# Kernel optimization log

Measured on AMD Instinct MI355X. Metric: run time of the kernel, lower is better.

Reference implementation:

```python
import jax, jax.numpy as jnp
import numpy as np

N_NODES = 100000
N_EDGES = 1600000
HIDDEN = 64


def gcn_conv(x, edge_index, W, b):
    """PyG GCNConv: add self-loops, symmetric deg^{-1/2} normalization, scatter-add."""
    n = x.shape[0]
    h = x @ W  # [N, F_out]
    loop = jnp.arange(n, dtype=edge_index.dtype)
    src = jnp.concatenate([edge_index[0], loop])  # [E+N]
    dst = jnp.concatenate([edge_index[1], loop])
    deg = jax.ops.segment_sum(jnp.ones_like(dst, dtype=h.dtype), dst, num_segments=n)
    dinv = jnp.where(deg > 0, jax.lax.rsqrt(jnp.maximum(deg, 1e-12)), 0.0)
    norm = dinv[src] * dinv[dst]  # [E+N]
    msg = h[src] * norm[:, None]  # gather + scale
    out = jax.ops.segment_sum(msg, dst, num_segments=n)  # scatter-add
    return out + b


def setup_inputs() -> dict:
    key = jax.random.key(0)
    k = jax.random.split(key, 6)
    x = jax.random.normal(k[0], (N_NODES, HIDDEN), dtype=jnp.float32)
    edge_index = jax.random.randint(k[1], (2, N_EDGES), 0, N_NODES, dtype=jnp.int32)
    s = 1.0 / np.sqrt(HIDDEN)
    W1 = jax.random.normal(k[2], (HIDDEN, HIDDEN), dtype=jnp.float32) * s
    b1 = jnp.zeros((HIDDEN,), dtype=jnp.float32)
    W2 = jax.random.normal(k[3], (HIDDEN, HIDDEN), dtype=jnp.float32) * s
    b2 = jnp.zeros((HIDDEN,), dtype=jnp.float32)
    return {"x": x, "edge_index": edge_index, "W1": W1, "b1": b1, "W2": W2, "b2": b2}


def reference(x, edge_index, W1, b1, W2, b2):
    # Faithful to source: conv1 applied twice, relu, dropout (eval -> identity), conv2, log_softmax.
    h = gcn_conv(x, edge_index, W1, b1)
    h = jax.nn.relu(gcn_conv(h, edge_index, W1, b1))
    # F.dropout(training=self.training): identity in eval mode
    h = gcn_conv(h, edge_index, W2, b2)
    return jax.nn.log_softmax(h, axis=1)
```

## Files before the change

### kernel.cpp

```cpp
#include <hip/hip_runtime.h>
#include <hip/hip_bf16.h>

#define HID 64

__device__ __forceinline__ void acc8(float* a, uint4 v) {
    a[0] += __uint_as_float(v.x << 16);
    a[1] += __uint_as_float(v.x & 0xffff0000u);
    a[2] += __uint_as_float(v.y << 16);
    a[3] += __uint_as_float(v.y & 0xffff0000u);
    a[4] += __uint_as_float(v.z << 16);
    a[5] += __uint_as_float(v.z & 0xffff0000u);
    a[6] += __uint_as_float(v.w << 16);
    a[7] += __uint_as_float(v.w & 0xffff0000u);
}


__global__ __launch_bounds__(256) void hist_part_kernel(
    const int* __restrict__ dst, int* __restrict__ cnt, int E, int psz) {
    int part = blockIdx.x & 7, chunk = blockIdx.x >> 3;
    int i = chunk * 256 + threadIdx.x;
    if (i >= E) return;
    int d = dst[i];
    if (d / psz == part) atomicAdd(&cnt[d], 1);
}

__global__ __launch_bounds__(256) void bsum_kernel(const int* __restrict__ cnt,
                                                   int* __restrict__ bsums, int N) {
    __shared__ int s[256];
    int tid = threadIdx.x, i = blockIdx.x * 256 + tid;
    s[tid] = (i < N) ? cnt[i] : 0;
    __syncthreads();
    for (int o = 128; o > 0; o >>= 1) {
        if (tid < o) s[tid] += s[tid + o];
        __syncthreads();
    }
    if (tid == 0) bsums[blockIdx.x] = s[0];
}

__global__ __launch_bounds__(512) void scan_bsums_kernel(int* __restrict__ bsums, int nblk) {
    __shared__ int s[512];
    int tid = threadIdx.x;
    int orig = (tid < nblk) ? bsums[tid] : 0;
    s[tid] = orig;
    __syncthreads();
    for (int off = 1; off < 512; off <<= 1) {
        int v = (tid >= off) ? s[tid - off] : 0;
        __syncthreads();
        s[tid] += v;
        __syncthreads();
    }
    if (tid < nblk) bsums[tid] = s[tid] - orig;
}

__global__ __launch_bounds__(256) void rowptr_kernel(
    const int* __restrict__ cnt, const int* __restrict__ bsums,
    int* __restrict__ row_ptr, int* __restrict__ cursor,
    float* __restrict__ dinv, int N) {
    __shared__ int s[256];
    int tid = threadIdx.x, i = blockIdx.x * 256 + tid;
    int c = (i < N) ? cnt[i] : 0;
    s[tid] = c;
    __syncthreads();
    for (int off = 1; off < 256; off <<= 1) {
        int v = (tid >= off) ? s[tid - off] : 0;
        __syncthreads();
        s[tid] += v;
        __syncthreads();
    }
    if (i < N) {
        int excl = s[tid] - c + bsums[blockIdx.x];
        row_ptr[i] = excl;
        cursor[i]  = excl;
        dinv[i]    = rsqrtf((float)c + 1.0f);
    }
}

__global__ __launch_bounds__(256) void fill_part_kernel(
    const int* __restrict__ src, const int* __restrict__ dst,
    int* __restrict__ cursor, int* __restrict__ col, int E, int psz) {
    int part = blockIdx.x & 7, chunk = blockIdx.x >> 3;
    int i = chunk * 256 + threadIdx.x;
    if (i >= E) return;
    int d = dst[i];
    if (d / psz == part) {
        int p = atomicAdd(&cursor[d], 1);
        col[p] = src[i];
    }
}

__device__ __forceinline__ void gather64(
    const uint4* __restrict__ g4, const int* __restrict__ col,
    int beg, int deg, int n, int N, int lane, float* t) {
    int eighth = lane >> 3, fo = lane & 7;
    float a0[8] = {}, a1[8] = {}, a2[8] = {}, a3[8] = {};
    for (int base = 0; base < deg; base += 64) {
        int rem = deg - base; rem = rem > 64 ? 64 : rem;
        int c = (lane < rem) ? col[beg + base + lane] : N;
        int groups = (rem + 7) >> 3;
        int j = 0;
        for (; j + 4 <= groups; j += 4) {
            int s0 = __shfl(c, 8 * (j + 0) + eighth, 64);
            int s1 = __shfl(c, 8 * (j + 1) + eighth, 64);
            int s2 = __shfl(c, 8 * (j + 2) + eighth, 64);
            int s3 = __shfl(c, 8 * (j + 3) + eighth, 64);
            uint4 v0 = g4[(size_t)s0 * 8 + fo];
            uint4 v1 = g4[(size_t)s1 * 8 + fo];
            uint4 v2 = g4[(size_t)s2 * 8 + fo];
            uint4 v3 = g4[(size_t)s3 * 8 + fo];
            acc8(a0, v0); acc8(a1, v1); acc8(a2, v2); acc8(a3, v3);
        }
        if (j + 2 <= groups) {
            int s0 = __shfl(c, 8 * (j + 0) + eighth, 64);
            int s1 = __shfl(c, 8 * (j + 1) + eighth, 64);
            uint4 v0 = g4[(size_t)s0 * 8 + fo];
            uint4 v1 = g4[(size_t)s1 * 8 + fo];
            acc8(a0, v0); acc8(a1, v1);
            j += 2;
        }
        if (j < groups) {
            int s0 = __shfl(c, 8 * j + eighth, 64);
            uint4 v0 = g4[(size_t)s0 * 8 + fo];
            acc8(a0, v0);
        }
    }
    float sf[8] = {};
    acc8(sf, g4[(size_t)n * 8 + fo]);
#pragma unroll
    for (int k = 0; k < 8; ++k) {
        float s = (a0[k] + a1[k]) + (a2[k] + a3[k]);
        s += __shfl_xor(s, 8, 64);
        s += __shfl_xor(s, 16, 64);
        s += __shfl_xor(s, 32, 64);
        t[k] = s + sf[k];
    }
}


__global__ __launch_bounds__(256) void gemm_scale_kernel(
    const float* __restrict__ X, const float* __restrict__ W,
    const float* __restrict__ dinv, __hip_bfloat16* __restrict__ g, int N) {
    __shared__ float Ws[HID * HID];
    __shared__ float4 xs4[4][HID / 4];
    int tid = threadIdx.x;
    for (int i = tid; i < HID * HID; i += 256) Ws[i] = W[i];
    __syncthreads();
    int w = tid >> 6, c = tid & 63;
    float* xsw = (float*)xs4[w];
    int ngrp = (N + 4) / 4;
    for (int grp = blockIdx.x; grp < ngrp; grp += gridDim.x) {
        int row = grp * 4 + w;
        if (row > N) continue;
        if (row == N) { g[(size_t)N * HID + c] = __float2bfloat16(0.f); continue; }
        xsw[c] = X[(size_t)row * HID + c];
        float acc = 0.f;
#pragma unroll
        for (int k = 0; k < HID; ++k) acc = fmaf(xsw[k], Ws[k * HID + c], acc);
        g[(size_t)row * HID + c] = __float2bfloat16(acc * dinv[row]);
    }
}


template <bool RELU>
__global__ __launch_bounds__(256) void agg_gemm_kernel(
    const __hip_bfloat16* __restrict__ g_in, const int* __restrict__ row_ptr,
    const int* __restrict__ cnt, const int* __restrict__ col,
    const float* __restrict__ dinv, const float* __restrict__ bias,
    const float* __restrict__ W, __hip_bfloat16* __restrict__ g_out, int N) {
    __shared__ float Ws[HID * HID];
    __shared__ float4 xs4[4][HID / 4];
    int tid = threadIdx.x;
    for (int i = tid; i < HID * HID; i += 256) Ws[i] = W[i];
    __syncthreads();
    int w = tid >> 6, lane = tid & 63;
    int eighth = lane >> 3, fo = lane & 7;
    const uint4* g4 = (const uint4*)g_in;
    float* xsw = (float*)xs4[w];
    float bb[8];
#pragma unroll
    for (int k = 0; k < 8; ++k) bb[k] = bias[8 * fo + k];
    int ngrp = (N + 4) / 4;
    for (int grp = blockIdx.x; grp < ngrp; grp += gridDim.x) {
        int n = grp * 4 + w;
        if (n > N) continue;
        if (n == N) { g_out[(size_t)N * HID + lane] = __float2bfloat16(0.f); continue; }
        int beg = __builtin_amdgcn_readfirstlane(row_ptr[n]);
        int deg = __builtin_amdgcn_readfirstlane(cnt[n]);
        float dn = __uint_as_float(__builtin_amdgcn_readfirstlane(__float_as_uint(dinv[n])));
        float t[8];
        gather64(g4, col, beg, deg, n, N, lane, t);
        if (eighth == 0) {
            float4 o0, o1;
            o0.x = fmaf(dn, t[0], bb[0]); o0.y = fmaf(dn, t[1], bb[1]);
            o0.z = fmaf(dn, t[2], bb[2]); o0.w = fmaf(dn, t[3], bb[3]);
            o1.x = fmaf(dn, t[4], bb[4]); o1.y = fmaf(dn, t[5], bb[5]);
            o1.z = fmaf(dn, t[6], bb[6]); o1.w = fmaf(dn, t[7], bb[7]);
            if (RELU) {
                o0.x = fmaxf(o0.x, 0.f); o0.y = fmaxf(o0.y, 0.f);
                o0.z = fmaxf(o0.z, 0.f); o0.w = fmaxf(o0.w, 0.f);
                o1.x = fmaxf(o1.x, 0.f); o1.y = fmaxf(o1.y, 0.f);
                o1.z = fmaxf(o1.z, 0.f); o1.w = fmaxf(o1.w, 0.f);
            }
            xs4[w][2 * fo]     = o0;
            xs4[w][2 * fo + 1] = o1;
        }
        float acc = 0.f;
#pragma unroll
        for (int k = 0; k < HID; ++k) acc = fmaf(xsw[k], Ws[k * HID + lane], acc);
        g_out[(size_t)n * HID + lane] = __float2bfloat16(acc * dn);
    }
}


__global__ __launch_bounds__(256) void agg_lsm_kernel(
    const __hip_bfloat16* __restrict__ g_in, const int* __restrict__ row_ptr,
    const int* __restrict__ cnt, const int* __restrict__ col,
    const float* __restrict__ dinv, const float* __restrict__ bias,
    float* __restrict__ out, int N) {
    int tid = threadIdx.x;
    int n = blockIdx.x * 4 + (tid >> 6);
    if (n >= N) return;
    int lane = tid & 63;
    int eighth = lane >> 3, fo = lane & 7;
    int beg = __builtin_amdgcn_readfirstlane(row_ptr[n]);
    int deg = __builtin_amdgcn_readfirstlane(cnt[n]);
    float dn = __uint_as_float(__builtin_amdgcn_readfirstlane(__float_as_uint(dinv[n])));
    const uint4* g4 = (const uint4*)g_in;
    float t[8];
    gather64(g4, col, beg, deg, n, N, lane, t);
    float v[8];
#pragma unroll
    for (int k = 0; k < 8; ++k) v[k] = fmaf(dn, t[k], bias[8 * fo + k]);
    float mx = v[0];
#pragma unroll
    for (int k = 1; k < 8; ++k) mx = fmaxf(mx, v[k]);
    mx = fmaxf(mx, __shfl_xor(mx, 1, 64));
    mx = fmaxf(mx, __shfl_xor(mx, 2, 64));
    mx = fmaxf(mx, __shfl_xor(mx, 4, 64));
    float sum = 0.f;
#pragma unroll
    for (int k = 0; k < 8; ++k) sum += expf(v[k] - mx);
    sum += __shfl_xor(sum, 1, 64);
    sum += __shfl_xor(sum, 2, 64);
    sum += __shfl_xor(sum, 4, 64);
    float ls = mx + logf(sum);
    if (eighth == 0) {
        float4 o0 = make_float4(v[0] - ls, v[1] - ls, v[2] - ls, v[3] - ls);
        float4 o1 = make_float4(v[4] - ls, v[5] - ls, v[6] - ls, v[7] - ls);
        ((float4*)out)[(size_t)n * 16 + 2 * fo]     = o0;
        ((float4*)out)[(size_t)n * 16 + 2 * fo + 1] = o1;
    }
}


static inline size_t alignup(size_t x) { return (x + 255) & ~(size_t)255; }

extern "C" void kernel_launch(void* const* d_in, const int* in_sizes, int n_in,
                              void* d_out, int out_size, void* d_ws, size_t ws_size,
                              hipStream_t stream) {
    const float* x  = (const float*)d_in[0];
    const int*   ei = (const int*)d_in[1];
    const float* W1 = (const float*)d_in[2];
    const float* b1 = (const float*)d_in[3];
    const float* W2 = (const float*)d_in[4];
    const float* b2 = (const float*)d_in[5];

    const int N = in_sizes[0] / HID;
    const int E = in_sizes[1] / 2;
    const int* src = ei;
    const int* dst = ei + E;

    const int nblk = (N + 255) / 256;
    const int psz  = (N + 7) / 8;

    char* w = (char*)d_ws;
    float*          dinv    = (float*)w;          w += alignup((size_t)N * 4);
    __hip_bfloat16* gA      = (__hip_bfloat16*)w; w += alignup((size_t)(N + 1) * HID * 2);
    __hip_bfloat16* gB      = (__hip_bfloat16*)w; w += alignup((size_t)(N + 1) * HID * 2);
    int*            cnt     = (int*)w;            w += alignup((size_t)N * 4);
    int*            row_ptr = (int*)w;            w += alignup((size_t)N * 4);
    int*            cursor  = (int*)w;            w += alignup((size_t)N * 4);
    int*            col     = (int*)w;            w += alignup((size_t)E * 4);
    int*            bsums   = (int*)w;            w += alignup((size_t)nblk * 4);

    const int egrid = (E + 255) / 256;
    const int ngrid = (N + 3) / 4;
    const int gsgrid = 2048;

    hipMemsetAsync(cnt, 0, (size_t)N * sizeof(int), stream);
    hist_part_kernel<<<egrid * 8, 256, 0, stream>>>(dst, cnt, E, psz);
    bsum_kernel<<<nblk, 256, 0, stream>>>(cnt, bsums, N);
    scan_bsums_kernel<<<1, 512, 0, stream>>>(bsums, nblk);
    rowptr_kernel<<<nblk, 256, 0, stream>>>(cnt, bsums, row_ptr, cursor, dinv, N);
    fill_part_kernel<<<egrid * 8, 256, 0, stream>>>(src, dst, cursor, col, E, psz);

    gemm_scale_kernel<<<gsgrid, 256, 0, stream>>>(x, W1, dinv, gA, N);
    agg_gemm_kernel<false><<<gsgrid, 256, 0, stream>>>(gA, row_ptr, cnt, col, dinv, b1, W1, gB, N);
    agg_gemm_kernel<true><<<gsgrid, 256, 0, stream>>>(gB, row_ptr, cnt, col, dinv, b1, W2, gA, N);
    agg_lsm_kernel<<<ngrid, 256, 0, stream>>>(gA, row_ptr, cnt, col, dinv, b2, (float*)d_out, N);
}
```

Before: 405.8 us.

## Pack node metadata, keep weights in registers, use nontemporal memory ops

```diff
diff --git a/kernel.cpp b/kernel.cpp
--- a/kernel.cpp
+++ b/kernel.cpp
@@ -3,6 +3,12 @@
 
 #define HID 64
 
+typedef float f32x4 __attribute__((ext_vector_type(4)));
+
+__device__ __forceinline__ unsigned short f2bf(float f) {
+    unsigned u = __float_as_uint(f);
+    return (unsigned short)((u + 0x7fffu + ((u >> 16) & 1u)) >> 16);
+}
 __device__ __forceinline__ void acc8(float* a, uint4 v) {
     a[0] += __uint_as_float(v.x << 16);
     a[1] += __uint_as_float(v.x & 0xffff0000u);
@@ -20,7 +26,7 @@
     int part = blockIdx.x & 7, chunk = blockIdx.x >> 3;
     int i = chunk * 256 + threadIdx.x;
     if (i >= E) return;
-    int d = dst[i];
+    int d = __builtin_nontemporal_load(&dst[i]);
     if (d / psz == part) atomicAdd(&cnt[d], 1);
 }
 
@@ -54,8 +60,7 @@
 
 __global__ __launch_bounds__(256) void rowptr_kernel(
     const int* __restrict__ cnt, const int* __restrict__ bsums,
-    int* __restrict__ row_ptr, int* __restrict__ cursor,
-    float* __restrict__ dinv, int N) {
+    int4* __restrict__ nodeinfo, int* __restrict__ cursor, int N) {
     __shared__ int s[256];
     int tid = threadIdx.x, i = blockIdx.x * 256 + tid;
     int c = (i < N) ? cnt[i] : 0;
@@ -69,9 +74,13 @@
     }
     if (i < N) {
         int excl = s[tid] - c + bsums[blockIdx.x];
-        row_ptr[i] = excl;
-        cursor[i]  = excl;
-        dinv[i]    = rsqrtf((float)c + 1.0f);
+        cursor[i] = excl;
+        int4 ni;
+        ni.x = excl;
+        ni.y = c;
+        ni.z = (int)__float_as_uint(rsqrtf((float)c + 1.0f));
+        ni.w = 0;
+        nodeinfo[i] = ni;
     }
 }
 
@@ -81,10 +90,11 @@
     int part = blockIdx.x & 7, chunk = blockIdx.x >> 3;
     int i = chunk * 256 + threadIdx.x;
     if (i >= E) return;
-    int d = dst[i];
+    int d = __builtin_nontemporal_load(&dst[i]);
     if (d / psz == part) {
+        int s = __builtin_nontemporal_load(&src[i]);
         int p = atomicAdd(&cursor[d], 1);
-        col[p] = src[i];
+        __builtin_nontemporal_store(s, &col[p]);
     }
 }
 
@@ -92,30 +102,18 @@
     const uint4* __restrict__ g4, const int* __restrict__ col,
     int beg, int deg, int n, int N, int lane, float* t) {
     int eighth = lane >> 3, fo = lane & 7;
-    float a0[8] = {}, a1[8] = {}, a2[8] = {}, a3[8] = {};
+    float a0[8] = {}, a1[8] = {};
     for (int base = 0; base < deg; base += 64) {
         int rem = deg - base; rem = rem > 64 ? 64 : rem;
-        int c = (lane < rem) ? col[beg + base + lane] : N;
+        int c = (lane < rem) ? __builtin_nontemporal_load(&col[beg + base + lane]) : N;
         int groups = (rem + 7) >> 3;
         int j = 0;
-        for (; j + 4 <= groups; j += 4) {
-            int s0 = __shfl(c, 8 * (j + 0) + eighth, 64);
-            int s1 = __shfl(c, 8 * (j + 1) + eighth, 64);
-            int s2 = __shfl(c, 8 * (j + 2) + eighth, 64);
-            int s3 = __shfl(c, 8 * (j + 3) + eighth, 64);
-            uint4 v0 = g4[(size_t)s0 * 8 + fo];
-            uint4 v1 = g4[(size_t)s1 * 8 + fo];
-            uint4 v2 = g4[(size_t)s2 * 8 + fo];
-            uint4 v3 = g4[(size_t)s3 * 8 + fo];
-            acc8(a0, v0); acc8(a1, v1); acc8(a2, v2); acc8(a3, v3);
-        }
-        if (j + 2 <= groups) {
+        for (; j + 2 <= groups; j += 2) {
             int s0 = __shfl(c, 8 * (j + 0) + eighth, 64);
             int s1 = __shfl(c, 8 * (j + 1) + eighth, 64);
             uint4 v0 = g4[(size_t)s0 * 8 + fo];
             uint4 v1 = g4[(size_t)s1 * 8 + fo];
             acc8(a0, v0); acc8(a1, v1);
-            j += 2;
         }
         if (j < groups) {
             int s0 = __shfl(c, 8 * j + eighth, 64);
@@ -127,7 +125,7 @@
     acc8(sf, g4[(size_t)n * 8 + fo]);
 #pragma unroll
     for (int k = 0; k < 8; ++k) {
-        float s = (a0[k] + a1[k]) + (a2[k] + a3[k]);
+        float s = a0[k] + a1[k];
         s += __shfl_xor(s, 8, 64);
         s += __shfl_xor(s, 16, 64);
         s += __shfl_xor(s, 32, 64);
@@ -138,92 +136,81 @@
 
 __global__ __launch_bounds__(256) void gemm_scale_kernel(
     const float* __restrict__ X, const float* __restrict__ W,
-    const float* __restrict__ dinv, __hip_bfloat16* __restrict__ g, int N) {
-    __shared__ float Ws[HID * HID];
-    __shared__ float4 xs4[4][HID / 4];
-    int tid = threadIdx.x;
-    for (int i = tid; i < HID * HID; i += 256) Ws[i] = W[i];
-    __syncthreads();
-    int w = tid >> 6, c = tid & 63;
-    float* xsw = (float*)xs4[w];
+    const int4* __restrict__ nodeinfo, unsigned short* __restrict__ g, int N) {
+    int tid = threadIdx.x, w = tid >> 6, lane = tid & 63;
+    float Wreg[64];
+#pragma unroll
+    for (int k = 0; k < HID; ++k) Wreg[k] = W[k * HID + lane];
     int ngrp = (N + 4) / 4;
     for (int grp = blockIdx.x; grp < ngrp; grp += gridDim.x) {
         int row = grp * 4 + w;
         if (row > N) continue;
-        if (row == N) { g[(size_t)N * HID + c] = __float2bfloat16(0.f); continue; }
-        xsw[c] = X[(size_t)row * HID + c];
+        if (row == N) { __builtin_nontemporal_store((unsigned short)0, &g[(size_t)N * HID + lane]); continue; }
+        float xv = __builtin_nontemporal_load(&X[(size_t)row * HID + lane]);
+        float dn = __uint_as_float(__builtin_amdgcn_readfirstlane((unsigned)nodeinfo[row].z));
         float acc = 0.f;
 #pragma unroll
-        for (int k = 0; k < HID; ++k) acc = fmaf(xsw[k], Ws[k * HID + c], acc);
-        g[(size_t)row * HID + c] = __float2bfloat16(acc * dinv[row]);
+        for (int k = 0; k < HID; ++k) acc = fmaf(__shfl(xv, k, 64), Wreg[k], acc);
+        __builtin_nontemporal_store(f2bf(acc * dn), &g[(size_t)row * HID + lane]);
     }
 }
 
 
 template <bool RELU>
 __global__ __launch_bounds__(256) void agg_gemm_kernel(
-    const __hip_bfloat16* __restrict__ g_in, const int* __restrict__ row_ptr,
-    const int* __restrict__ cnt, const int* __restrict__ col,
-    const float* __restrict__ dinv, const float* __restrict__ bias,
-    const float* __restrict__ W, __hip_bfloat16* __restrict__ g_out, int N) {
-    __shared__ float Ws[HID * HID];
-    __shared__ float4 xs4[4][HID / 4];
-    int tid = threadIdx.x;
-    for (int i = tid; i < HID * HID; i += 256) Ws[i] = W[i];
-    __syncthreads();
-    int w = tid >> 6, lane = tid & 63;
-    int eighth = lane >> 3, fo = lane & 7;
+    const unsigned short* __restrict__ g_in, const int4* __restrict__ nodeinfo,
+    const int* __restrict__ col, const float* __restrict__ bias,
+    const float* __restrict__ W, unsigned short* __restrict__ g_out, int N) {
+    int tid = threadIdx.x, w = tid >> 6, lane = tid & 63;
+    int fo = lane & 7;
+    float Wreg[64];
+#pragma unroll
+    for (int k = 0; k < HID; ++k) Wreg[k] = W[k * HID + lane];
+    float bb[8];
+#pragma unroll
+    for (int j = 0; j < 8; ++j) bb[j] = bias[8 * fo + j];
     const uint4* g4 = (const uint4*)g_in;
-    float* xsw = (float*)xs4[w];
-    float bb[8];
-#pragma unroll
-    for (int k = 0; k < 8; ++k) bb[k] = bias[8 * fo + k];
     int ngrp = (N + 4) / 4;
     for (int grp = blockIdx.x; grp < ngrp; grp += gridDim.x) {
         int n = grp * 4 + w;
         if (n > N) continue;
-        if (n == N) { g_out[(size_t)N * HID + lane] = __float2bfloat16(0.f); continue; }
-        int beg = __builtin_amdgcn_readfirstlane(row_ptr[n]);
-        int deg = __builtin_amdgcn_readfirstlane(cnt[n]);
-        float dn = __uint_as_float(__builtin_amdgcn_readfirstlane(__float_as_uint(dinv[n])));
+        if (n == N) { __builtin_nontemporal_store((unsigned short)0, &g_out[(size_t)N * HID + lane]); continue; }
+        int4 ni = nodeinfo[n];
+        int beg  = __builtin_amdgcn_readfirstlane(ni.x);
+        int deg  = __builtin_amdgcn_readfirstlane(ni.y);
+        float dn = __uint_as_float(__builtin_amdgcn_readfirstlane((unsigned)ni.z));
         float t[8];
         gather64(g4, col, beg, deg, n, N, lane, t);
-        if (eighth == 0) {
-            float4 o0, o1;
-            o0.x = fmaf(dn, t[0], bb[0]); o0.y = fmaf(dn, t[1], bb[1]);
-            o0.z = fmaf(dn, t[2], bb[2]); o0.w = fmaf(dn, t[3], bb[3]);
-            o1.x = fmaf(dn, t[4], bb[4]); o1.y = fmaf(dn, t[5], bb[5]);
-            o1.z = fmaf(dn, t[6], bb[6]); o1.w = fmaf(dn, t[7], bb[7]);
-            if (RELU) {
-                o0.x = fmaxf(o0.x, 0.f); o0.y = fmaxf(o0.y, 0.f);
-                o0.z = fmaxf(o0.z, 0.f); o0.w = fmaxf(o0.w, 0.f);
-                o1.x = fmaxf(o1.x, 0.f); o1.y = fmaxf(o1.y, 0.f);
-                o1.z = fmaxf(o1.z, 0.f); o1.w = fmaxf(o1.w, 0.f);
-            }
-            xs4[w][2 * fo]     = o0;
-            xs4[w][2 * fo + 1] = o1;
+        float o[8];
+#pragma unroll
+        for (int j = 0; j < 8; ++j) {
+            o[j] = fmaf(dn, t[j], bb[j]);
+            if (RELU) o[j] = fmaxf(o[j], 0.f);
         }
         float acc = 0.f;
 #pragma unroll
-        for (int k = 0; k < HID; ++k) acc = fmaf(xsw[k], Ws[k * HID + lane], acc);
-        g_out[(size_t)n * HID + lane] = __float2bfloat16(acc * dn);
+        for (int q = 0; q < 8; ++q)
+#pragma unroll
+            for (int j = 0; j < 8; ++j)
+                acc = fmaf(__shfl(o[j], q, 64), Wreg[8 * q + j], acc);
+        __builtin_nontemporal_store(f2bf(acc * dn), &g_out[(size_t)n * HID + lane]);
     }
 }
 
 
 __global__ __launch_bounds__(256) void agg_lsm_kernel(
-    const __hip_bfloat16* __restrict__ g_in, const int* __restrict__ row_ptr,
-    const int* __restrict__ cnt, const int* __restrict__ col,
-    const float* __restrict__ dinv, const float* __restrict__ bias,
+    const unsigned short* __restrict__ g_in, const int4* __restrict__ nodeinfo,
+    const int* __restrict__ col, const float* __restrict__ bias,
     float* __restrict__ out, int N) {
     int tid = threadIdx.x;
     int n = blockIdx.x * 4 + (tid >> 6);
     if (n >= N) return;
     int lane = tid & 63;
     int eighth = lane >> 3, fo = lane & 7;
-    int beg = __builtin_amdgcn_readfirstlane(row_ptr[n]);
-    int deg = __builtin_amdgcn_readfirstlane(cnt[n]);
-    float dn = __uint_as_float(__builtin_amdgcn_readfirstlane(__float_as_uint(dinv[n])));
+    int4 ni = nodeinfo[n];
+    int beg  = __builtin_amdgcn_readfirstlane(ni.x);
+    int deg  = __builtin_amdgcn_readfirstlane(ni.y);
+    float dn = __uint_as_float(__builtin_amdgcn_readfirstlane((unsigned)ni.z));
     const uint4* g4 = (const uint4*)g_in;
     float t[8];
     gather64(g4, col, beg, deg, n, N, lane, t);
@@ -244,10 +231,11 @@
     sum += __shfl_xor(sum, 4, 64);
     float ls = mx + logf(sum);
     if (eighth == 0) {
-        float4 o0 = make_float4(v[0] - ls, v[1] - ls, v[2] - ls, v[3] - ls);
-        float4 o1 = make_float4(v[4] - ls, v[5] - ls, v[6] - ls, v[7] - ls);
-        ((float4*)out)[(size_t)n * 16 + 2 * fo]     = o0;
-        ((float4*)out)[(size_t)n * 16 + 2 * fo + 1] = o1;
+        f32x4 o0 = {v[0] - ls, v[1] - ls, v[2] - ls, v[3] - ls};
+        f32x4 o1 = {v[4] - ls, v[5] - ls, v[6] - ls, v[7] - ls};
+        f32x4* op = (f32x4*)out;
+        __builtin_nontemporal_store(o0, &op[(size_t)n * 16 + 2 * fo]);
+        __builtin_nontemporal_store(o1, &op[(size_t)n * 16 + 2 * fo + 1]);
     }
 }
 
@@ -273,28 +261,27 @@
     const int psz  = (N + 7) / 8;
 
     char* w = (char*)d_ws;
-    float*          dinv    = (float*)w;          w += alignup((size_t)N * 4);
-    __hip_bfloat16* gA      = (__hip_bfloat16*)w; w += alignup((size_t)(N + 1) * HID * 2);
-    __hip_bfloat16* gB      = (__hip_bfloat16*)w; w += alignup((size_t)(N + 1) * HID * 2);
-    int*            cnt     = (int*)w;            w += alignup((size_t)N * 4);
-    int*            row_ptr = (int*)w;            w += alignup((size_t)N * 4);
-    int*            cursor  = (int*)w;            w += alignup((size_t)N * 4);
-    int*            col     = (int*)w;            w += alignup((size_t)E * 4);
-    int*            bsums   = (int*)w;            w += alignup((size_t)nblk * 4);
-
-    const int egrid = (E + 255) / 256;
-    const int ngrid = (N + 3) / 4;
+    unsigned short* gA       = (unsigned short*)w; w += alignup((size_t)(N + 1) * HID * 2);
+    unsigned short* gB       = (unsigned short*)w; w += alignup((size_t)(N + 1) * HID * 2);
+    int4*           nodeinfo = (int4*)w;           w += alignup((size_t)N * 16);
+    int*            cnt      = (int*)w;            w += alignup((size_t)N * 4);
+    int*            cursor   = (int*)w;            w += alignup((size_t)N * 4);
+    int*            col      = (int*)w;            w += alignup((size_t)E * 4);
+    int*            bsums    = (int*)w;            w += alignup((size_t)nblk * 4);
+
+    const int egrid  = (E + 255) / 256;
+    const int ngrid  = (N + 3) / 4;
     const int gsgrid = 2048;
 
-    hipMemsetAsync(cnt, 0, (size_t)N * sizeof(int), stream);
+    (void)hipMemsetAsync(cnt, 0, (size_t)N * sizeof(int), stream);
     hist_part_kernel<<<egrid * 8, 256, 0, stream>>>(dst, cnt, E, psz);
     bsum_kernel<<<nblk, 256, 0, stream>>>(cnt, bsums, N);
     scan_bsums_kernel<<<1, 512, 0, stream>>>(bsums, nblk);
-    rowptr_kernel<<<nblk, 256, 0, stream>>>(cnt, bsums, row_ptr, cursor, dinv, N);
+    rowptr_kernel<<<nblk, 256, 0, stream>>>(cnt, bsums, nodeinfo, cursor, N);
     fill_part_kernel<<<egrid * 8, 256, 0, stream>>>(src, dst, cursor, col, E, psz);
 
-    gemm_scale_kernel<<<gsgrid, 256, 0, stream>>>(x, W1, dinv, gA, N);
-    agg_gemm_kernel<false><<<gsgrid, 256, 0, stream>>>(gA, row_ptr, cnt, col, dinv, b1, W1, gB, N);
-    agg_gemm_kernel<true><<<gsgrid, 256, 0, stream>>>(gB, row_ptr, cnt, col, dinv, b1, W2, gA, N);
-    agg_lsm_kernel<<<ngrid, 256, 0, stream>>>(gA, row_ptr, cnt, col, dinv, b2, (float*)d_out, N);
-}
+    gemm_scale_kernel<<<gsgrid, 256, 0, stream>>>(x, W1, nodeinfo, gA, N);
+    agg_gemm_kernel<false><<<gsgrid, 256, 0, stream>>>(gA, nodeinfo, col, b1, W1, gB, N);
+    agg_gemm_kernel<true><<<gsgrid, 256, 0, stream>>>(gB, nodeinfo, col, b1, W2, gA, N);
+    agg_lsm_kernel<<<ngrid, 256, 0, stream>>>(gA, nodeinfo, col, b2, (float*)d_out, N);
+}
```

Measured after the change: 498.1 us. +22.7%, slower.
